# Kernel tuning notes

Measured on AMD Instinct MI355X. Metric: run time of the kernel, lower is better.

The kernel has to match this reference:

```python
import jax, jax.numpy as jnp
import numpy as np

B, T, C, H = 4, 4096, 1024, 64

def setup_inputs() -> dict:
    key = jax.random.key(0)
    kx, kq, kk, kv = jax.random.split(key, 4)
    x  = jax.random.normal(kx, (B, T, C), dtype=jnp.float32)
    # nn.Linear(C, H, bias=False) weights have shape [H, C]; y = x @ W.T
    Wq = jax.random.normal(kq, (H, C), dtype=jnp.float32) * (C ** -0.5)
    Wk = jax.random.normal(kk, (H, C), dtype=jnp.float32) * (C ** -0.5)
    Wv = jax.random.normal(kv, (H, C), dtype=jnp.float32) * (C ** -0.5)
    return {"x": x, "Wq": Wq, "Wk": Wk, "Wv": Wv}

def reference(x, Wq, Wk, Wv):
    T_ = x.shape[1]
    scale = jnp.asarray(Wq.shape[0] ** -0.5, dtype=x.dtype)
    q = jnp.einsum('btc,hc->bth', x, Wq)
    k = jnp.einsum('btc,hc->bth', x, Wk)
    v = jnp.einsum('btc,hc->bth', x, Wv)
    w = jnp.einsum('bqh,bkh->bqk', q, k)  # [B, T, T] scores
    causal = jnp.tril(jnp.ones((T_, T_), dtype=bool))
    # original: masked_fill(-inf) then scale; -inf * scale == -inf, so equivalent
    w = jnp.where(causal, w * scale, -jnp.inf)
    w = jax.nn.softmax(w, axis=-1)
    # dropout p=0.0 (eval/deterministic): identity
    return jnp.einsum('bqk,bkh->bqh', w, v)
```

## Files before the change

kernel.cpp:

```cpp
#include <hip/hip_runtime.h>
#include <hip/hip_bf16.h>

#define B_ 4
#define T_ 4096
#define C_ 1024

typedef __bf16 bf16_t;
typedef __bf16 bf16x8 __attribute__((ext_vector_type(8)));
typedef float f32x4 __attribute__((ext_vector_type(4)));

__device__ __forceinline__ void gld16(const void* g, void* l) {
    __builtin_amdgcn_global_load_lds((const __attribute__((address_space(1))) void*)g,
                                     (__attribute__((address_space(3))) void*)l, 16, 0, 0);
}

__global__ void wcvt_kernel(const float* __restrict__ Wq, const float* __restrict__ Wk,
                            const float* __restrict__ Wv, bf16_t* __restrict__ wbf) {
    int i = blockIdx.x * 256 + threadIdx.x;
    int m = i >> 16;
    int r = i & 65535;
    const float* src = (m == 0) ? Wq : (m == 1) ? Wk : Wv;
    float s = (m == 0) ? 0.125f * 1.44269504f : 1.0f;
    wbf[i] = (bf16_t)(src[r] * s);
}

__global__ __launch_bounds__(256, 3)
void qkv_proj_kernel(const float* __restrict__ x, const bf16_t* __restrict__ wbf,
                     bf16_t* __restrict__ qb, bf16_t* __restrict__ kb,
                     bf16_t* __restrict__ vtb) {
    __shared__ float  xs[3][1024];
    __shared__ bf16_t wsb[3][6144];

    const int tid = threadIdx.x;
    const int w = tid >> 6, lane = tid & 63, lr = lane & 15, kg = lane >> 4;
    const int rg = w & 1, cg = w >> 1;
    const int row0 = blockIdx.x * 32;

#define STAGE_X(kk, sl) {                                                           \
        int r = tid >> 3, u = tid & 7;                                              \
        gld16((const char*)x + (size_t)(row0 + r) * 4096 + (size_t)(kk) * 128       \
                  + ((u ^ (r & 7)) * 16),                                           \
              (char*)&xs[sl][0] + (size_t)tid * 16); }
#define STAGE_W(kk, sl) {                                                           \
        _Pragma("unroll")                                                           \
        for (int j = 0; j < 3; ++j) {                                               \
            int idx = tid + j * 256; int h = idx >> 2, u = idx & 3;                 \
            gld16((const char*)wbf + (size_t)h * 2048 + (size_t)(kk) * 64           \
                      + ((u ^ (h & 3)) * 16),                                       \
                  (char*)&wsb[sl][0] + (size_t)idx * 16); } }

    f32x4 acc[6];
    #pragma unroll
    for (int j = 0; j < 6; ++j) acc[j] = (f32x4){0.f, 0.f, 0.f, 0.f};

    STAGE_X(0, 0); STAGE_W(0, 0);
    STAGE_X(1, 1); STAGE_W(1, 1);

    #pragma unroll
    for (int c = 0; c < 32; ++c) {
        if (c < 31) {
            asm volatile("s_waitcnt vmcnt(4)" ::: "memory");
        } else {
            asm volatile("s_waitcnt vmcnt(0)" ::: "memory");
        }
        __builtin_amdgcn_s_barrier();
        if (c + 2 < 32) {
            STAGE_X(c + 2, (c + 2) % 3);
            STAGE_W(c + 2, (c + 2) % 3);
        }

        {
            const int sl = c % 3;
            const int rl = rg * 16 + lr;
            const float* xrow = &xs[sl][rl * 32];
            float4 f0 = *(const float4*)(xrow + (((kg * 2)     ^ (lr & 7)) * 4));
            float4 f1 = *(const float4*)(xrow + (((kg * 2 + 1) ^ (lr & 7)) * 4));
            bf16x8 af;
            af[0]=(bf16_t)f0.x; af[1]=(bf16_t)f0.y; af[2]=(bf16_t)f0.z; af[3]=(bf16_t)f0.w;
            af[4]=(bf16_t)f1.x; af[5]=(bf16_t)f1.y; af[6]=(bf16_t)f1.z; af[7]=(bf16_t)f1.w;

            __builtin_amdgcn_s_setprio(1);
            #pragma unroll
            for (int j = 0; j < 6; ++j) {
                int h = (cg * 6 + j) * 16 + lr;
                bf16x8 bfr = *(const bf16x8*)&wsb[sl][h * 32 + ((kg ^ (lr & 3)) * 8)];
                acc[j] = __builtin_amdgcn_mfma_f32_16x16x32_bf16(af, bfr, acc[j], 0, 0, 0);
            }
            __builtin_amdgcn_s_setprio(0);
        }
    }

    #pragma unroll
    for (int j = 0; j < 6; ++j) {
        int p = cg * 6 + j;
        int m = p >> 2;
        int h = (p & 3) * 16 + lr;
        #pragma unroll
        for (int i = 0; i < 4; ++i) {
            int t = row0 + rg * 16 + kg * 4 + i;
            float v = acc[j][i];
            if (m == 0) {
                qb[(size_t)t * 64 + h] = (bf16_t)v;
            } else if (m == 1) {
                kb[(size_t)t * 64 + ((((h >> 3) ^ (t & 7)) << 3) | (h & 7))] = (bf16_t)v;
            } else {
                int bb = t >> 12, tt = t & 4095;
                vtb[(size_t)(bb * 64 + h) * 4096 + (tt & ~63)
                    + (((((tt >> 3) & 7) ^ (h & 7))) << 3) + (tt & 7)] = (bf16_t)v;
            }
        }
    }
#undef STAGE_X
#undef STAGE_W
}

__global__ __launch_bounds__(256, 2)
void attn_kernel(const bf16_t* __restrict__ qb, const bf16_t* __restrict__ kb,
                 const bf16_t* __restrict__ vtb, float* __restrict__ out) {
    __shared__ bf16_t kvb[2][2][8192];
    __shared__ bf16_t p_lds[4][16][68];

    const int tid = threadIdx.x;
    const int w = tid >> 6, lane = tid & 63, lr = lane & 15, kg = lane >> 4;
    const int rg = w & 1, slice = w >> 1;
    const int bid = blockIdx.x;
    const int b = bid & 3;
    const int qt = 127 - (bid >> 2);
    const int qrow0 = qt * 32 + rg * 16;
    const size_t bT = (size_t)b * 4096;

    const int nch    = (qt + 2) >> 1;
    const int nsteps = (nch + 1) >> 1;

#define STAGE_CHUNK(kk, pp, cc) {                                                   \
        _Pragma("unroll")                                                           \
        for (int jj = 0; jj < 2; ++jj) {                                            \
            int idx = tid + jj * 256;                                               \
            gld16((const char*)kb + (bT + (size_t)(kk) * 64) * 128 + (size_t)idx * 16, \
                  (char*)&kvb[pp][cc][0] + (size_t)idx * 16);                       \
            gld16((const char*)vtb + (size_t)(b * 64 + (idx >> 3)) * 8192           \
                      + (size_t)(kk) * 128 + (idx & 7) * 16,                        \
                  (char*)&kvb[pp][cc][4096] + (size_t)idx * 16); } }
#define STAGE_PAIR(j1) {                                                            \
        int c0 = 2 * (j1), c1 = 2 * (j1) + 1, pp = (j1) & 1;                        \
        if (c0 < nch) STAGE_CHUNK(c0, pp, 0);                                       \
        if (c1 < nch) STAGE_CHUNK(c1, pp, 1); }

    bf16x8 qf[2];
    #pragma unroll
    for (int s = 0; s < 2; ++s)
        qf[s] = *(const bf16x8*)&qb[(bT + qrow0 + lr) * 64 + s * 32 + kg * 8];

    f32x4 o_acc[4];
    float l_i[4];
    #pragma unroll
    for (int ct = 0; ct < 4; ++ct) o_acc[ct] = (f32x4){0.f, 0.f, 0.f, 0.f};
    #pragma unroll
    for (int i = 0; i < 4; ++i) l_i[i] = 0.f;

    STAGE_PAIR(0);

    for (int j = 0; j < nsteps; ++j) {
        asm volatile("s_waitcnt vmcnt(0)" ::: "memory");
        __builtin_amdgcn_s_barrier();
        asm volatile("" ::: "memory");
        if (j + 1 < nsteps) STAGE_PAIR(j + 1);

        int c = 2 * j + slice;
        if (c < nch) {
            const bf16_t* Kt = &kvb[j & 1][slice][0];
            const bf16_t* Vt = &kvb[j & 1][slice][4096];
            int kv0 = c * 64;

            f32x4 sc[4];
            #pragma unroll
            for (int ct = 0; ct < 4; ++ct) sc[ct] = (f32x4){0.f, 0.f, 0.f, 0.f};
            __builtin_amdgcn_s_setprio(1);
            #pragma unroll
            for (int ct = 0; ct < 4; ++ct)
                #pragma unroll
                for (int s = 0; s < 2; ++s) {
                    bf16x8 kf = *(const bf16x8*)&Kt[(ct * 16 + lr) * 64 + (((kg + 4 * s) ^ (lr & 7)) * 8)];
                    sc[ct] = __builtin_amdgcn_mfma_f32_16x16x32_bf16(qf[s], kf, sc[ct], 0, 0, 0);
                }
            __builtin_amdgcn_s_setprio(0);

            if (kv0 + 63 > qrow0) {
                #pragma unroll
                for (int ct = 0; ct < 4; ++ct)
                    #pragma unroll
                    for (int i = 0; i < 4; ++i) {
                        int col = kv0 + ct * 16 + lr;
                        int rw  = qrow0 + kg * 4 + i;
                        if (col > rw) sc[ct][i] = -INFINITY;
                    }
            }

            #pragma unroll
            for (int ct = 0; ct < 4; ++ct)
                #pragma unroll
                for (int i = 0; i < 4; ++i) {
                    float p = __builtin_amdgcn_exp2f(sc[ct][i]);
                    p_lds[w][kg * 4 + i][ct * 16 + lr] = (bf16_t)p;
                    l_i[i] += p;
                }

            bf16x8 pf[2];
            #pragma unroll
            for (int s = 0; s < 2; ++s)
                pf[s] = *(const bf16x8*)&p_lds[w][lr][s * 32 + kg * 8];
            __builtin_amdgcn_s_setprio(1);
            #pragma unroll
            for (int ct = 0; ct < 4; ++ct)
                #pragma unroll
                for (int s = 0; s < 2; ++s) {
                    bf16x8 vf = *(const bf16x8*)&Vt[(ct * 16 + lr) * 64 + (((kg + 4 * s) ^ (lr & 7)) * 8)];
                    o_acc[ct] = __builtin_amdgcn_mfma_f32_16x16x32_bf16(pf[s], vf, o_acc[ct], 0, 0, 0);
                }
            __builtin_amdgcn_s_setprio(0);
        }
    }

    asm volatile("s_waitcnt vmcnt(0)" ::: "memory");
    __syncthreads();

    #pragma unroll
    for (int off = 1; off < 16; off <<= 1)
        #pragma unroll
        for (int i = 0; i < 4; ++i)
            l_i[i] += __shfl_xor(l_i[i], off);

    float* co = (float*)&kvb[0][0][0];
    float* cl = co + 2 * 16 * 66;
    if (slice == 1) {
        #pragma unroll
        for (int ct = 0; ct < 4; ++ct)
            #pragma unroll
            for (int i = 0; i < 4; ++i)
                co[(rg * 16 + kg * 4 + i) * 66 + ct * 16 + lr] = o_acc[ct][i];
        if (lr == 0) {
            #pragma unroll
            for (int i = 0; i < 4; ++i)
                cl[rg * 16 + kg * 4 + i] = l_i[i];
        }
    }
    __syncthreads();
    if (slice == 0) {
        #pragma unroll
        for (int i = 0; i < 4; ++i) {
            int r = kg * 4 + i;
            float lv = l_i[i] + cl[rg * 16 + r];
            float inv = 1.0f / lv;
            #pragma unroll
            for (int ct = 0; ct < 4; ++ct) {
                float ov = o_acc[ct][i] + co[(rg * 16 + r) * 66 + ct * 16 + lr];
                out[(bT + qrow0 + r) * 64 + ct * 16 + lr] = ov * inv;
            }
        }
    }
#undef STAGE_CHUNK
#undef STAGE_PAIR
}

extern "C" void kernel_launch(void* const* d_in, const int* in_sizes, int n_in,
                              void* d_out, int out_size, void* d_ws, size_t ws_size,
                              hipStream_t stream) {
    const float* x  = (const float*)d_in[0];
    const float* Wq = (const float*)d_in[1];
    const float* Wk = (const float*)d_in[2];
    const float* Wv = (const float*)d_in[3];
    float* out = (float*)d_out;

    bf16_t* ws  = (bf16_t*)d_ws;
    bf16_t* wbf = ws;
    bf16_t* qb  = ws + 196608;
    bf16_t* kb  = qb + 1048576;
    bf16_t* vtb = kb + 1048576;

    wcvt_kernel<<<768, 256, 0, stream>>>(Wq, Wk, Wv, wbf);
    qkv_proj_kernel<<<512, 256, 0, stream>>>(x, wbf, qb, kb, vtb);
    attn_kernel<<<512, 256, 0, stream>>>(qb, kb, vtb, out);
}
```

Measured before the change: 67.23 us.

## Double K-chunk size in QKV projection with split X/W prefetch pipeline

The projection kernel now consumes 64-wide K chunks (16 iterations instead of 32), giving two MFMAs per weight tile per iteration and halving barriers. X keeps a triple-buffer prefetched two steps ahead while W is double-buffered one step ahead, with pointer rotation and the loop left rolled. LDS per block roughly doubles, so occupancy hint drops from 3 to 2 blocks per CU, risking less latency hiding.

```diff
diff --git a/kernel.cpp b/kernel.cpp
--- a/kernel.cpp
+++ b/kernel.cpp
@@ -24,70 +24,90 @@
     wbf[i] = (bf16_t)(src[r] * s);
 }
 
-__global__ __launch_bounds__(256, 3)
+__global__ __launch_bounds__(256, 2)
 void qkv_proj_kernel(const float* __restrict__ x, const bf16_t* __restrict__ wbf,
                      bf16_t* __restrict__ qb, bf16_t* __restrict__ kb,
                      bf16_t* __restrict__ vtb) {
-    __shared__ float  xs[3][1024];
-    __shared__ bf16_t wsb[3][6144];
+    __shared__ float  xs[3][2048];
+    __shared__ bf16_t wsb[2][12288];
 
     const int tid = threadIdx.x;
     const int w = tid >> 6, lane = tid & 63, lr = lane & 15, kg = lane >> 4;
     const int rg = w & 1, cg = w >> 1;
     const int row0 = blockIdx.x * 32;
 
-#define STAGE_X(kk, sl) {                                                           \
-        int r = tid >> 3, u = tid & 7;                                              \
-        gld16((const char*)x + (size_t)(row0 + r) * 4096 + (size_t)(kk) * 128       \
-                  + ((u ^ (r & 7)) * 16),                                           \
-              (char*)&xs[sl][0] + (size_t)tid * 16); }
-#define STAGE_W(kk, sl) {                                                           \
+    const int xr_ = tid >> 4, xu = tid & 15;
+    const char* xg = (const char*)x + (size_t)(row0 + xr_) * 4096
+                     + (((xu >> 1) ^ (xr_ & 7)) * 32) + ((xu & 1) * 16);
+    const int wh = tid >> 3, wu = tid & 7;
+    const char* wg = (const char*)wbf;
+
+    char* xs_c  = (char*)&xs[0][0];
+    char* xs_n  = (char*)&xs[1][0];
+    char* xs_nn = (char*)&xs[2][0];
+    char* ws_c  = (char*)&wsb[0][0];
+    char* ws_n  = (char*)&wsb[1][0];
+
+#define ISSUE_X(kk, dst) {                                                          \
+        gld16(xg + (size_t)(kk) * 256,         (dst) + (size_t)tid * 16);           \
+        gld16(xg + 65536 + (size_t)(kk) * 256, (dst) + 4096 + (size_t)tid * 16); }
+#define ISSUE_W(kk, dst) {                                                          \
         _Pragma("unroll")                                                           \
-        for (int j = 0; j < 3; ++j) {                                               \
-            int idx = tid + j * 256; int h = idx >> 2, u = idx & 3;                 \
-            gld16((const char*)wbf + (size_t)h * 2048 + (size_t)(kk) * 64           \
-                      + ((u ^ (h & 3)) * 16),                                       \
-                  (char*)&wsb[sl][0] + (size_t)idx * 16); } }
+        for (int j = 0; j < 6; ++j) {                                               \
+            int h = wh + j * 32;                                                    \
+            gld16(wg + (size_t)h * 2048 + (size_t)(kk) * 128 + ((wu ^ (h & 7)) * 16), \
+                  (dst) + (size_t)(tid + j * 256) * 16); } }
 
     f32x4 acc[6];
     #pragma unroll
     for (int j = 0; j < 6; ++j) acc[j] = (f32x4){0.f, 0.f, 0.f, 0.f};
 
-    STAGE_X(0, 0); STAGE_W(0, 0);
-    STAGE_X(1, 1); STAGE_W(1, 1);
-
-    #pragma unroll
-    for (int c = 0; c < 32; ++c) {
-        if (c < 31) {
-            asm volatile("s_waitcnt vmcnt(4)" ::: "memory");
+    ISSUE_X(0, xs_c);
+    ISSUE_W(0, ws_c);
+    ISSUE_X(1, xs_n);
+
+    const int rl = rg * 16 + lr;
+    const int xoff0 = (((kg)     ^ (lr & 7)) * 32);
+    const int xoff1 = (((kg + 4) ^ (lr & 7)) * 32);
+
+    #pragma clang loop unroll(disable)
+    for (int c = 0; c < 16; ++c) {
+        if (c < 15) {
+            asm volatile("s_waitcnt vmcnt(2)" ::: "memory");
         } else {
             asm volatile("s_waitcnt vmcnt(0)" ::: "memory");
         }
         __builtin_amdgcn_s_barrier();
-        if (c + 2 < 32) {
-            STAGE_X(c + 2, (c + 2) % 3);
-            STAGE_W(c + 2, (c + 2) % 3);
-        }
+        if (c < 15) ISSUE_W(c + 1, ws_n);
+        if (c < 14) ISSUE_X(c + 2, xs_nn);
 
         {
-            const int sl = c % 3;
-            const int rl = rg * 16 + lr;
-            const float* xrow = &xs[sl][rl * 32];
-            float4 f0 = *(const float4*)(xrow + (((kg * 2)     ^ (lr & 7)) * 4));
-            float4 f1 = *(const float4*)(xrow + (((kg * 2 + 1) ^ (lr & 7)) * 4));
-            bf16x8 af;
-            af[0]=(bf16_t)f0.x; af[1]=(bf16_t)f0.y; af[2]=(bf16_t)f0.z; af[3]=(bf16_t)f0.w;
-            af[4]=(bf16_t)f1.x; af[5]=(bf16_t)f1.y; af[6]=(bf16_t)f1.z; af[7]=(bf16_t)f1.w;
+            const char* xrow = xs_c + (size_t)rl * 256;
+            float4 a0 = *(const float4*)(xrow + xoff0);
+            float4 a1 = *(const float4*)(xrow + xoff0 + 16);
+            float4 b0 = *(const float4*)(xrow + xoff1);
+            float4 b1 = *(const float4*)(xrow + xoff1 + 16);
+            bf16x8 af0, af1;
+            af0[0]=(bf16_t)a0.x; af0[1]=(bf16_t)a0.y; af0[2]=(bf16_t)a0.z; af0[3]=(bf16_t)a0.w;
+            af0[4]=(bf16_t)a1.x; af0[5]=(bf16_t)a1.y; af0[6]=(bf16_t)a1.z; af0[7]=(bf16_t)a1.w;
+            af1[0]=(bf16_t)b0.x; af1[1]=(bf16_t)b0.y; af1[2]=(bf16_t)b0.z; af1[3]=(bf16_t)b0.w;
+            af1[4]=(bf16_t)b1.x; af1[5]=(bf16_t)b1.y; af1[6]=(bf16_t)b1.z; af1[7]=(bf16_t)b1.w;
 
             __builtin_amdgcn_s_setprio(1);
             #pragma unroll
             for (int j = 0; j < 6; ++j) {
                 int h = (cg * 6 + j) * 16 + lr;
-                bf16x8 bfr = *(const bf16x8*)&wsb[sl][h * 32 + ((kg ^ (lr & 3)) * 8)];
-                acc[j] = __builtin_amdgcn_mfma_f32_16x16x32_bf16(af, bfr, acc[j], 0, 0, 0);
+                const char* wrow = ws_c + (size_t)h * 128;
+                bf16x8 w0 = *(const bf16x8*)(wrow + (((kg)     ^ (lr & 7)) * 16));
+                bf16x8 w1 = *(const bf16x8*)(wrow + (((kg + 4) ^ (lr & 7)) * 16));
+                acc[j] = __builtin_amdgcn_mfma_f32_16x16x32_bf16(af0, w0, acc[j], 0, 0, 0);
+                acc[j] = __builtin_amdgcn_mfma_f32_16x16x32_bf16(af1, w1, acc[j], 0, 0, 0);
             }
             __builtin_amdgcn_s_setprio(0);
         }
+
+        char* tx = xs_c; xs_c = xs_n; xs_n = xs_nn; xs_nn = tx;
+        char* tw = ws_c; ws_c = ws_n; ws_n = tw;
     }
 
     #pragma unroll
@@ -110,8 +130,8 @@
             }
         }
     }
-#undef STAGE_X
-#undef STAGE_W
+#undef ISSUE_X
+#undef ISSUE_W
 }
 
 __global__ __launch_bounds__(256, 2)
```

After: 70.65 us. 5.1% more time.

## Rewrite QKV projection to hold x rows in registers and stream weights

Applied to the files above, without the earlier changes.

The QKV projection kernel drops its LDS-staged, barrier-synchronized pipeline. Each wave now converts its 16 rows of x to bf16 once and keeps all 1024 columns in registers. It then loops over 12 output tiles, double-buffering the weight fragments from global memory in registers, so there are no LDS traffic or block barriers. The grid is halved to 64 rows per block. The cost is very high VGPR use: 96 bf16x8 arrays means 384 VGPRs, which lowers occupancy, and the weights are reread per wave from global memory or L2 instead of being shared through LDS.

```diff
diff --git a/kernel.cpp b/kernel.cpp
--- a/kernel.cpp
+++ b/kernel.cpp
@@ -24,94 +24,71 @@
     wbf[i] = (bf16_t)(src[r] * s);
 }
 
-__global__ __launch_bounds__(256, 3)
+__global__ __launch_bounds__(256)
 void qkv_proj_kernel(const float* __restrict__ x, const bf16_t* __restrict__ wbf,
                      bf16_t* __restrict__ qb, bf16_t* __restrict__ kb,
                      bf16_t* __restrict__ vtb) {
-    __shared__ float  xs[3][1024];
-    __shared__ bf16_t wsb[3][6144];
-
     const int tid = threadIdx.x;
     const int w = tid >> 6, lane = tid & 63, lr = lane & 15, kg = lane >> 4;
-    const int rg = w & 1, cg = w >> 1;
-    const int row0 = blockIdx.x * 32;
-
-#define STAGE_X(kk, sl) {                                                           \
-        int r = tid >> 3, u = tid & 7;                                              \
-        gld16((const char*)x + (size_t)(row0 + r) * 4096 + (size_t)(kk) * 128       \
-                  + ((u ^ (r & 7)) * 16),                                           \
-              (char*)&xs[sl][0] + (size_t)tid * 16); }
-#define STAGE_W(kk, sl) {                                                           \
-        _Pragma("unroll")                                                           \
-        for (int j = 0; j < 3; ++j) {                                               \
-            int idx = tid + j * 256; int h = idx >> 2, u = idx & 3;                 \
-            gld16((const char*)wbf + (size_t)h * 2048 + (size_t)(kk) * 64           \
-                      + ((u ^ (h & 3)) * 16),                                       \
-                  (char*)&wsb[sl][0] + (size_t)idx * 16); } }
-
-    f32x4 acc[6];
-    #pragma unroll
-    for (int j = 0; j < 6; ++j) acc[j] = (f32x4){0.f, 0.f, 0.f, 0.f};
-
-    STAGE_X(0, 0); STAGE_W(0, 0);
-    STAGE_X(1, 1); STAGE_W(1, 1);
-
+    const int row0 = blockIdx.x * 64 + w * 16;
+
+    const float* xr = x + (size_t)(row0 + lr) * 1024 + kg * 8;
+    bf16x8 xreg[32];
     #pragma unroll
     for (int c = 0; c < 32; ++c) {
-        if (c < 31) {
-            asm volatile("s_waitcnt vmcnt(4)" ::: "memory");
-        } else {
-            asm volatile("s_waitcnt vmcnt(0)" ::: "memory");
-        }
-        __builtin_amdgcn_s_barrier();
-        if (c + 2 < 32) {
-            STAGE_X(c + 2, (c + 2) % 3);
-            STAGE_W(c + 2, (c + 2) % 3);
-        }
-
-        {
-            const int sl = c % 3;
-            const int rl = rg * 16 + lr;
-            const float* xrow = &xs[sl][rl * 32];
-            float4 f0 = *(const float4*)(xrow + (((kg * 2)     ^ (lr & 7)) * 4));
-            float4 f1 = *(const float4*)(xrow + (((kg * 2 + 1) ^ (lr & 7)) * 4));
-            bf16x8 af;
-            af[0]=(bf16_t)f0.x; af[1]=(bf16_t)f0.y; af[2]=(bf16_t)f0.z; af[3]=(bf16_t)f0.w;
-            af[4]=(bf16_t)f1.x; af[5]=(bf16_t)f1.y; af[6]=(bf16_t)f1.z; af[7]=(bf16_t)f1.w;
-
-            __builtin_amdgcn_s_setprio(1);
-            #pragma unroll
-            for (int j = 0; j < 6; ++j) {
-                int h = (cg * 6 + j) * 16 + lr;
-                bf16x8 bfr = *(const bf16x8*)&wsb[sl][h * 32 + ((kg ^ (lr & 3)) * 8)];
-                acc[j] = __builtin_amdgcn_mfma_f32_16x16x32_bf16(af, bfr, acc[j], 0, 0, 0);
-            }
-            __builtin_amdgcn_s_setprio(0);
-        }
-    }
-
-    #pragma unroll
-    for (int j = 0; j < 6; ++j) {
-        int p = cg * 6 + j;
-        int m = p >> 2;
-        int h = (p & 3) * 16 + lr;
-        #pragma unroll
-        for (int i = 0; i < 4; ++i) {
-            int t = row0 + rg * 16 + kg * 4 + i;
-            float v = acc[j][i];
-            if (m == 0) {
-                qb[(size_t)t * 64 + h] = (bf16_t)v;
-            } else if (m == 1) {
-                kb[(size_t)t * 64 + ((((h >> 3) ^ (t & 7)) << 3) | (h & 7))] = (bf16_t)v;
-            } else {
-                int bb = t >> 12, tt = t & 4095;
-                vtb[(size_t)(bb * 64 + h) * 4096 + (tt & ~63)
-                    + (((((tt >> 3) & 7) ^ (h & 7))) << 3) + (tt & 7)] = (bf16_t)v;
-            }
-        }
-    }
-#undef STAGE_X
-#undef STAGE_W
+        float4 a0 = *(const float4*)(xr + c * 32);
+        float4 a1 = *(const float4*)(xr + c * 32 + 4);
+        bf16x8 v;
+        v[0]=(bf16_t)a0.x; v[1]=(bf16_t)a0.y; v[2]=(bf16_t)a0.z; v[3]=(bf16_t)a0.w;
+        v[4]=(bf16_t)a1.x; v[5]=(bf16_t)a1.y; v[6]=(bf16_t)a1.z; v[7]=(bf16_t)a1.w;
+        xreg[c] = v;
+    }
+
+    const bf16_t* wp = wbf + (size_t)lr * 1024 + kg * 8;
+
+    bf16x8 wA[32], wB[32];
+    f32x4 acc;
+
+#define LOADW(p, buf) {                                                             \
+        _Pragma("unroll")                                                           \
+        for (int c = 0; c < 32; ++c)                                                \
+            buf[c] = *(const bf16x8*)(wp + (size_t)(p) * 16384 + c * 32); }
+#define DOMFMA(buf) {                                                               \
+        acc = (f32x4){0.f, 0.f, 0.f, 0.f};                                          \
+        _Pragma("unroll")                                                           \
+        for (int c = 0; c < 32; ++c)                                                \
+            acc = __builtin_amdgcn_mfma_f32_16x16x32_bf16(xreg[c], buf[c], acc, 0, 0, 0); }
+#define STORE(p) {                                                                  \
+        const int m = (p) >> 2;                                                     \
+        const int h = ((p) & 3) * 16 + lr;                                          \
+        _Pragma("unroll")                                                           \
+        for (int i = 0; i < 4; ++i) {                                               \
+            int t = row0 + kg * 4 + i;                                              \
+            float v = acc[i];                                                       \
+            if (m == 0) {                                                           \
+                qb[(size_t)t * 64 + h] = (bf16_t)v;                                 \
+            } else if (m == 1) {                                                    \
+                kb[(size_t)t * 64 + ((((h >> 3) ^ (t & 7)) << 3) | (h & 7))] = (bf16_t)v; \
+            } else {                                                                \
+                int bb = t >> 12, tt = t & 4095;                                    \
+                vtb[(size_t)(bb * 64 + h) * 4096 + (tt & ~63)                       \
+                    + (((((tt >> 3) & 7) ^ (h & 7))) << 3) + (tt & 7)] = (bf16_t)v; \
+            }                                                                       \
+        } }
+
+    LOADW(0, wA);
+    #pragma unroll
+    for (int p = 0; p < 12; p += 2) {
+        LOADW(p + 1, wB);
+        DOMFMA(wA);
+        STORE(p);
+        if (p + 2 < 12) LOADW(p + 2, wA);
+        DOMFMA(wB);
+        STORE(p + 1);
+    }
+#undef LOADW
+#undef DOMFMA
+#undef STORE
 }
 
 __global__ __launch_bounds__(256, 2)
@@ -278,6 +255,6 @@
     bf16_t* vtb = kb + 1048576;
 
     wcvt_kernel<<<768, 256, 0, stream>>>(Wq, Wk, Wv, wbf);
-    qkv_proj_kernel<<<512, 256, 0, stream>>>(x, wbf, qb, kb, vtb);
+    qkv_proj_kernel<<<256, 256, 0, stream>>>(x, wbf, qb, kb, vtb);
     attn_kernel<<<512, 256, 0, stream>>>(qb, kb, vtb, out);
 }
```

After: 114.4 us. 1.7x slower.
